# Performance work log

Measured on AMD Instinct MI355X. Metric: run time of the kernel, lower is better.

The kernel has to match this reference:

```python
import jax, jax.numpy as jnp
import numpy as np
from jax import lax

EPS = 1e-5

def conv2d(x, w, groups=1, pad=0):
    return lax.conv_general_dilated(
        x, w, window_strides=(1, 1), padding=[(pad, pad), (pad, pad)],
        dimension_numbers=('NCHW', 'OIHW', 'NCHW'), feature_group_count=groups)

def setup_inputs() -> dict:
    key = jax.random.key(0)
    ks = jax.random.split(key, 10)
    B, C, H, W = 8, 64, 128, 128
    s = 0.05
    f32 = jnp.float32
    return {
        'x': jax.random.normal(ks[0], (B, C, H, W), f32),
        # key_embed: Conv2d(64,64,3,groups=8,bias=False) -> weight [64, 64/8, 3, 3]
        'w_key': jax.random.normal(ks[1], (64, 8, 3, 3), f32) * s,
        # embed[0]: Conv2d(128,32,1,groups=2,bias=False) -> [32, 128/2, 1, 1]
        'w_e1': jax.random.normal(ks[2], (32, 64, 1, 1), f32) * s,
        # embed[2]: Conv2d(32,72,1,groups=2,bias=True) -> [72, 32/2, 1, 1]
        'w_e2': jax.random.normal(ks[3], (72, 16, 1, 1), f32) * s,
        'b_e2': jax.random.normal(ks[4], (72,), f32) * s,
        # GroupNorm(num_groups=8, num_channels=72) affine params
        'gn_w': jnp.ones((72,), f32),
        'gn_b': jnp.zeros((72,), f32),
        # conv1x1: Conv2d(64,64,1,groups=2,bias=False) -> [64, 32, 1, 1]
        'w_c1': jax.random.normal(ks[5], (64, 32, 1, 1), f32) * s,
        # conv_du: Conv2d(64,4,1,bias=False), Conv2d(4,64,1,bias=False)
        'w_du1': jax.random.normal(ks[6], (4, 64, 1, 1), f32) * s,
        'w_du2': jax.random.normal(ks[7], (64, 4, 1, 1), f32) * s,
    }

def reference(x, w_key, w_e1, w_e2, b_e2, gn_w, gn_b, w_c1, w_du1, w_du2):
    B, C, H, W = x.shape  # C == 64
    KK = 9                # kernel_size^2
    # key embedding: grouped 3x3 conv + ReLU
    k = jax.nn.relu(conv2d(x, w_key, groups=8, pad=1))
    # interleave x and k along channels: view of [B,64,2,H,W] -> [B,128,H,W]
    qk = jnp.stack([x, k], axis=2).reshape(B, 2 * C, H, W)
    # dynamic kernel generation (embed)
    w = jax.nn.relu(conv2d(qk, w_e1, groups=2))
    w = conv2d(w, w_e2, groups=2) + b_e2[None, :, None, None]  # [B,72,H,W]
    # GroupNorm(8, 72): normalize over (channels-in-group, H, W)
    wg = w.reshape(B, 8, 9, H, W)
    m = wg.mean(axis=(2, 3, 4), keepdims=True)
    v = wg.var(axis=(2, 3, 4), keepdims=True)
    w = ((wg - m) * lax.rsqrt(v + EPS)).reshape(B, 72, H, W)
    w = w * gn_w[None, :, None, None] + gn_b[None, :, None, None]
    # per-pixel kernels: [B*2, 4, 9, H, W]
    w = w.reshape(B * 2, 4, KK, H, W)
    # value path
    xv = conv2d(x, w_c1, groups=2).reshape(B * 2, 32, H, W)
    # unfold 3x3 patches with zero padding 1 -> [B*2, 32, 9, H, W]
    xp = jnp.pad(xv, ((0, 0), (0, 0), (1, 1), (1, 1)))
    patches = jnp.stack(
        [xp[:, :, i:i + H, j:j + W] for i in range(3) for j in range(3)], axis=2)
    # share_planes=8: 8 channels share each kernel -> [B*2, 4, 8, 9, H, W]
    patches = patches.reshape(B * 2, 4, 8, KK, H, W)
    out = jnp.einsum('bgckhw,bgkhw->bgchw', patches, w)  # local conv
    out = out.reshape(B, C, H, W)
    # channel attention
    y = out.mean(axis=(2, 3))                 # [B, 64]
    y = jax.nn.relu(y @ w_du1[:, :, 0, 0].T)  # [B, 4]
    y = jax.nn.sigmoid(y @ w_du2[:, :, 0, 0].T)  # [B, 64]
    return out * y[:, :, None, None]
```

## Files before the change

### kernel.cpp

```cpp
#include <hip/hip_runtime.h>
#include <math.h>

#define Hd 128
#define Wd 128
#define HW 16384

__device__ __forceinline__ float wred(float v) {
  #pragma unroll
  for (int o = 32; o > 0; o >>= 1) v += __shfl_down(v, o, 64);
  return v;
}

__global__ __launch_bounds__(256, 4) void k_fused(const float* __restrict__ x,
                                                  const float* __restrict__ wkey,
                                                  const float* __restrict__ we1,
                                                  const float* __restrict__ we2,
                                                  const float* __restrict__ be2,
                                                  const float* __restrict__ wc1,
                                                  float* __restrict__ xv,
                                                  float* __restrict__ wpre,
                                                  float* __restrict__ spart) {
  __shared__ float xt[8][18][24];
  __shared__ float sred2[4][8];
  const int tid = threadIdx.x;
  const int tx = tid & 15, ty = tid >> 4;
  const int b = blockIdx.y, s = blockIdx.z;
  const int h0 = (blockIdx.x >> 3) * 16, w0 = (blockIdx.x & 7) * 16;
  const int p = ((h0 + ty) << 7) + (w0 + tx);
  float xc[32], kc[32];
  #pragma unroll
  for (int g = 0; g < 4; ++g) {
    for (int i = tid; i < 8 * 324; i += 256) {
      int ch = i / 324, r = i - ch * 324;
      int yy = r / 18, xx = r - yy * 18;
      int gh = h0 + yy - 1, gw = w0 + xx - 1;
      float v = 0.f;
      if (gh >= 0 && gh < Hd && gw >= 0 && gw < Wd)
        v = x[((long)(b * 64 + 32 * s + 8 * g + ch) << 14) + (gh << 7) + gw];
      xt[ch][yy][xx] = v;
    }
    __syncthreads();
    float kacc[8] = {0.f, 0.f, 0.f, 0.f, 0.f, 0.f, 0.f, 0.f};
    const float* wg = wkey + (4 * s + g) * 576;
    #pragma unroll
    for (int ich = 0; ich < 8; ++ich) {
      float nb[9];
      #pragma unroll
      for (int rr = 0; rr < 3; ++rr)
        #pragma unroll
        for (int cc = 0; cc < 3; ++cc)
          nb[rr * 3 + cc] = xt[ich][ty + rr][tx + cc];
      xc[8 * g + ich] = nb[4];
      #pragma unroll
      for (int oc = 0; oc < 8; ++oc) {
        const float* wr = wg + oc * 72 + ich * 9;
        #pragma unroll
        for (int k9 = 0; k9 < 9; ++k9) kacc[oc] += wr[k9] * nb[k9];
      }
    }
    #pragma unroll
    for (int oc = 0; oc < 8; ++oc) kc[8 * g + oc] = fmaxf(kacc[oc], 0.f);
    __syncthreads();
  }
  #pragma unroll 4
  for (int o = 0; o < 32; ++o) {
    const float* wr = wc1 + (32 * s + o) * 32;
    float a = 0.f;
    #pragma unroll
    for (int j = 0; j < 32; ++j) a += wr[j] * xc[j];
    xv[((long)(b * 64 + 32 * s + o) << 14) + p] = a;
  }
  float w1a[16];
  #pragma unroll
  for (int o = 0; o < 16; ++o) {
    const float* wr = we1 + (16 * s + o) * 64;
    float a = 0.f;
    #pragma unroll
    for (int j = 0; j < 32; ++j) a += wr[2 * j] * xc[j] + wr[2 * j + 1] * kc[j];
    w1a[o] = fmaxf(a, 0.f);
  }
  #pragma unroll
  for (int gl = 0; gl < 4; ++gl) {
    float lgs = 0.f, lgq = 0.f;
    #pragma unroll
    for (int kk = 0; kk < 9; ++kk) {
      const int oc2 = 36 * s + gl * 9 + kk;
      const float* wr = we2 + oc2 * 16;
      float a = be2[oc2];
      #pragma unroll
      for (int ic = 0; ic < 16; ++ic) a += wr[ic] * w1a[ic];
      wpre[((long)(b * 72 + oc2) << 14) + p] = a;
      lgs += a;
      lgq += a * a;
    }
    float r1 = wred(lgs), r2 = wred(lgq);
    if ((tid & 63) == 0) {
      sred2[tid >> 6][2 * gl] = r1;
      sred2[tid >> 6][2 * gl + 1] = r2;
    }
  }
  __syncthreads();
  if (tid < 8) {
    float a = sred2[0][tid] + sred2[1][tid] + sred2[2][tid] + sred2[3][tid];
    spart[blockIdx.x * 128 + b * 16 + s * 8 + tid] = a;
  }
}

__global__ void k_gnstat(const float* __restrict__ spart, float* __restrict__ minv) {
  __shared__ float sred[128];
  const int t = threadIdx.x;
  float a = 0.f;
  #pragma unroll 8
  for (int r = 0; r < 64; ++r) a += spart[r * 128 + t];
  sred[t] = a;
  __syncthreads();
  if (t < 64) {
    const float N = 9.f * (float)HW;
    float s = sred[2 * t], q = sred[2 * t + 1];
    float m = s / N;
    float var = q / N - m * m;
    minv[2 * t] = m;
    minv[2 * t + 1] = rsqrtf(var + 1e-5f);
  }
}

__global__ __launch_bounds__(256) void k_local(const float* __restrict__ kxv,
                                               const float* __restrict__ wpre,
                                               const float* __restrict__ minv,
                                               const float* __restrict__ gnw,
                                               const float* __restrict__ gnb,
                                               float* __restrict__ out,
                                               float* __restrict__ part) {
  __shared__ float xt[8][34][24];
  const int tid = threadIdx.x;
  const int tx = tid & 15, ty = tid >> 4;
  const int z = blockIdx.z;
  const int b2 = z >> 2, g = z & 3;
  const int t = b2 & 1, b = b2 >> 1;
  const int h0 = blockIdx.y * 32, w0 = blockIdx.x * 16;
  for (int i = tid; i < 8 * 612; i += 256) {
    int ch = i / 612, r = i - ch * 612;
    int yy = r / 18, xx = r - yy * 18;
    int gh = h0 + yy - 1, gw = w0 + xx - 1;
    float v = 0.f;
    if (gh >= 0 && gh < Hd && gw >= 0 && gw < Wd)
      v = kxv[((long)(b2 * 32 + g * 8 + ch) << 14) + (gh << 7) + gw];
    xt[ch][yy][xx] = v;
  }
  __syncthreads();
  const int gg = 4 * t + g;
  const float m = minv[(b * 8 + gg) * 2];
  const float inv = minv[(b * 8 + gg) * 2 + 1];
  const int p0 = ((h0 + 2 * ty) << 7) + (w0 + tx);
  const int p1 = p0 + 128;
  float wn0[9], wn1[9];
  #pragma unroll
  for (int kk = 0; kk < 9; ++kk) {
    const int ch72 = 36 * t + 9 * g + kk;
    const long base = ((long)(b * 72 + ch72) << 14);
    const float sc = inv * gnw[ch72], sh = gnb[ch72] - m * inv * gnw[ch72];
    wn0[kk] = wpre[base + p0] * sc + sh;
    wn1[kk] = wpre[base + p1] * sc + sh;
  }
  const int prow = (blockIdx.y * 8 + blockIdx.x) * 4 + (tid >> 6);
  #pragma unroll
  for (int cc = 0; cc < 8; ++cc) {
    float nb[12];
    #pragma unroll
    for (int rr = 0; rr < 4; ++rr)
      #pragma unroll
      for (int ccol = 0; ccol < 3; ++ccol)
        nb[rr * 3 + ccol] = xt[cc][2 * ty + rr][tx + ccol];
    float o0 = 0.f, o1 = 0.f;
    #pragma unroll
    for (int dy = 0; dy < 3; ++dy)
      #pragma unroll
      for (int dx = 0; dx < 3; ++dx) {
        o0 += wn0[dy * 3 + dx] * nb[dy * 3 + dx];
        o1 += wn1[dy * 3 + dx] * nb[(dy + 1) * 3 + dx];
      }
    const int ch512 = b2 * 32 + g * 8 + cc;
    out[((long)ch512 << 14) + p0] = o0;
    out[((long)ch512 << 14) + p1] = o1;
    float os = wred(o0 + o1);
    if ((tid & 63) == 0) part[prow * 512 + ch512] = os;
  }
}

__global__ void k_ca(const float* __restrict__ part, const float* __restrict__ du1,
                     const float* __restrict__ du2, float* __restrict__ ys) {
  __shared__ float sy[8][64];
  __shared__ float sy4[8][4];
  const int tid = threadIdx.x;
  const int b = tid >> 6, c = tid & 63;
  float acc = 0.f;
  #pragma unroll 8
  for (int r = 0; r < 128; ++r) acc += part[r * 512 + tid];
  sy[b][c] = acc * (1.f / (float)HW);
  __syncthreads();
  if (tid < 32) {
    int bb = tid >> 2, j = tid & 3;
    float a = 0.f;
    for (int c2 = 0; c2 < 64; ++c2) a += sy[bb][c2] * du1[j * 64 + c2];
    sy4[bb][j] = fmaxf(a, 0.f);
  }
  __syncthreads();
  float z = 0.f;
  #pragma unroll
  for (int j = 0; j < 4; ++j) z += sy4[b][j] * du2[c * 4 + j];
  ys[tid] = 1.f / (1.f + expf(-z));
}

__global__ __launch_bounds__(256) void k_scale(float* __restrict__ out,
                                               const float* __restrict__ ys) {
  const long i4 = (long)blockIdx.x * 256 + threadIdx.x;
  const long e = i4 * 4;
  const int bc = (int)(e >> 14);
  const float s = ys[bc];
  float4* o = (float4*)out;
  float4 v = o[i4];
  v.x *= s; v.y *= s; v.z *= s; v.w *= s;
  o[i4] = v;
}

extern "C" void kernel_launch(void* const* d_in, const int* in_sizes, int n_in,
                              void* d_out, int out_size, void* d_ws, size_t ws_size,
                              hipStream_t stream) {
  const float* x    = (const float*)d_in[0];
  const float* wkey = (const float*)d_in[1];
  const float* we1  = (const float*)d_in[2];
  const float* we2  = (const float*)d_in[3];
  const float* be2  = (const float*)d_in[4];
  const float* gnw  = (const float*)d_in[5];
  const float* gnb  = (const float*)d_in[6];
  const float* wc1  = (const float*)d_in[7];
  const float* du1  = (const float*)d_in[8];
  const float* du2  = (const float*)d_in[9];
  float* out = (float*)d_out;
  float* ws = (float*)d_ws;

  float* kxv  = ws;
  float* wpre = ws + 8388608;
  float* part = ws + 17825792;
  float* spart = part;
  float* minv = part + 131072;
  float* ys   = minv + 128;

  k_fused<<<dim3(64, 8, 2), 256, 0, stream>>>(x, wkey, we1, we2, be2, wc1, kxv, wpre, spart);
  k_gnstat<<<1, 128, 0, stream>>>(spart, minv);
  k_local<<<dim3(8, 4, 64), 256, 0, stream>>>(kxv, wpre, minv, gnw, gnb, out, part);
  k_ca<<<1, 512, 0, stream>>>(part, du1, du2, ys);
  k_scale<<<8192, 256, 0, stream>>>(out, ys);
}
```

Measured before the change: 233.3 us.

## Store xv and wpre channel-last and fold GroupNorm stats into local conv

The intermediate value tensor xv and the pre-norm kernel tensor wpre are now stored pixel-major (channels last) instead of planar. k_fused writes xv with float4 vector stores, and k_local loads each pixel's 8 channels with two float4 loads. The separate single-block GroupNorm statistics kernel is removed: each k_local block reduces its own group's partial sums with a wavefront shuffle, which saves one launch and one serial dependency. Costs: the wpre stores and loads become strided scalar accesses of 36 floats per pixel, which may coalesce worse. The k_fused launch-bounds occupancy hint and the outer loop unroll are also dropped.

```diff
diff --git a/kernel.cpp b/kernel.cpp
--- a/kernel.cpp
+++ b/kernel.cpp
@@ -11,15 +11,15 @@
   return v;
 }
 
-__global__ __launch_bounds__(256, 4) void k_fused(const float* __restrict__ x,
-                                                  const float* __restrict__ wkey,
-                                                  const float* __restrict__ we1,
-                                                  const float* __restrict__ we2,
-                                                  const float* __restrict__ be2,
-                                                  const float* __restrict__ wc1,
-                                                  float* __restrict__ xv,
-                                                  float* __restrict__ wpre,
-                                                  float* __restrict__ spart) {
+__global__ __launch_bounds__(256) void k_fused(const float* __restrict__ x,
+                                               const float* __restrict__ wkey,
+                                               const float* __restrict__ we1,
+                                               const float* __restrict__ we2,
+                                               const float* __restrict__ be2,
+                                               const float* __restrict__ wc1,
+                                               float* __restrict__ xv,
+                                               float* __restrict__ wpre,
+                                               float* __restrict__ spart) {
   __shared__ float xt[8][18][24];
   __shared__ float sred2[4][8];
   const int tid = threadIdx.x;
@@ -28,7 +28,6 @@
   const int h0 = (blockIdx.x >> 3) * 16, w0 = (blockIdx.x & 7) * 16;
   const int p = ((h0 + ty) << 7) + (w0 + tx);
   float xc[32], kc[32];
-  #pragma unroll
   for (int g = 0; g < 4; ++g) {
     for (int i = tid; i < 8 * 324; i += 256) {
       int ch = i / 324, r = i - ch * 324;
@@ -62,13 +61,19 @@
     for (int oc = 0; oc < 8; ++oc) kc[8 * g + oc] = fmaxf(kacc[oc], 0.f);
     __syncthreads();
   }
-  #pragma unroll 4
-  for (int o = 0; o < 32; ++o) {
-    const float* wr = wc1 + (32 * s + o) * 32;
-    float a = 0.f;
-    #pragma unroll
-    for (int j = 0; j < 32; ++j) a += wr[j] * xc[j];
-    xv[((long)(b * 64 + 32 * s + o) << 14) + p] = a;
+  float* xvp = xv + ((long)(b * HW + p)) * 64 + 32 * s;
+  #pragma unroll
+  for (int o4 = 0; o4 < 8; ++o4) {
+    float va[4];
+    #pragma unroll
+    for (int oo = 0; oo < 4; ++oo) {
+      const float* wr = wc1 + (32 * s + 4 * o4 + oo) * 32;
+      float a = 0.f;
+      #pragma unroll
+      for (int j = 0; j < 32; ++j) a += wr[j] * xc[j];
+      va[oo] = a;
+    }
+    ((float4*)xvp)[o4] = make_float4(va[0], va[1], va[2], va[3]);
   }
   float w1a[16];
   #pragma unroll
@@ -79,6 +84,7 @@
     for (int j = 0; j < 32; ++j) a += wr[2 * j] * xc[j] + wr[2 * j + 1] * kc[j];
     w1a[o] = fmaxf(a, 0.f);
   }
+  float* wpp = wpre + ((long)(b * HW + p)) * 72 + 36 * s;
   #pragma unroll
   for (int gl = 0; gl < 4; ++gl) {
     float lgs = 0.f, lgq = 0.f;
@@ -89,7 +95,7 @@
       float a = be2[oc2];
       #pragma unroll
       for (int ic = 0; ic < 16; ++ic) a += wr[ic] * w1a[ic];
-      wpre[((long)(b * 72 + oc2) << 14) + p] = a;
+      wpp[gl * 9 + kk] = a;
       lgs += a;
       lgq += a * a;
     }
@@ -106,61 +112,65 @@
   }
 }
 
-__global__ void k_gnstat(const float* __restrict__ spart, float* __restrict__ minv) {
-  __shared__ float sred[128];
-  const int t = threadIdx.x;
-  float a = 0.f;
-  #pragma unroll 8
-  for (int r = 0; r < 64; ++r) a += spart[r * 128 + t];
-  sred[t] = a;
-  __syncthreads();
-  if (t < 64) {
-    const float N = 9.f * (float)HW;
-    float s = sred[2 * t], q = sred[2 * t + 1];
-    float m = s / N;
-    float var = q / N - m * m;
-    minv[2 * t] = m;
-    minv[2 * t + 1] = rsqrtf(var + 1e-5f);
-  }
-}
-
-__global__ __launch_bounds__(256) void k_local(const float* __restrict__ kxv,
+__global__ __launch_bounds__(256) void k_local(const float* __restrict__ xv,
                                                const float* __restrict__ wpre,
-                                               const float* __restrict__ minv,
+                                               const float* __restrict__ spart,
                                                const float* __restrict__ gnw,
                                                const float* __restrict__ gnb,
                                                float* __restrict__ out,
                                                float* __restrict__ part) {
   __shared__ float xt[8][34][24];
+  __shared__ float sminv[2];
   const int tid = threadIdx.x;
   const int tx = tid & 15, ty = tid >> 4;
   const int z = blockIdx.z;
   const int b2 = z >> 2, g = z & 3;
   const int t = b2 & 1, b = b2 >> 1;
+  const int gg = 4 * t + g;
   const int h0 = blockIdx.y * 32, w0 = blockIdx.x * 16;
-  for (int i = tid; i < 8 * 612; i += 256) {
-    int ch = i / 612, r = i - ch * 612;
-    int yy = r / 18, xx = r - yy * 18;
+  for (int i = tid; i < 612; i += 256) {
+    int yy = i / 18, xx = i - yy * 18;
     int gh = h0 + yy - 1, gw = w0 + xx - 1;
-    float v = 0.f;
-    if (gh >= 0 && gh < Hd && gw >= 0 && gw < Wd)
-      v = kxv[((long)(b2 * 32 + g * 8 + ch) << 14) + (gh << 7) + gw];
-    xt[ch][yy][xx] = v;
-  }
-  __syncthreads();
-  const int gg = 4 * t + g;
-  const float m = minv[(b * 8 + gg) * 2];
-  const float inv = minv[(b * 8 + gg) * 2 + 1];
+    float4 v0 = make_float4(0.f, 0.f, 0.f, 0.f), v1 = v0;
+    if (gh >= 0 && gh < Hd && gw >= 0 && gw < Wd) {
+      const float4* src = (const float4*)(xv + ((long)(b * HW) + (gh << 7) + gw) * 64 +
+                                          32 * t + 8 * g);
+      v0 = src[0];
+      v1 = src[1];
+    }
+    xt[0][yy][xx] = v0.x; xt[1][yy][xx] = v0.y; xt[2][yy][xx] = v0.z; xt[3][yy][xx] = v0.w;
+    xt[4][yy][xx] = v1.x; xt[5][yy][xx] = v1.y; xt[6][yy][xx] = v1.z; xt[7][yy][xx] = v1.w;
+  }
+  if (tid < 64) {
+    const float* sp = spart + tid * 128 + (b * 8 + gg) * 2;
+    float sv = sp[0], qv = sp[1];
+    #pragma unroll
+    for (int o = 32; o > 0; o >>= 1) {
+      sv += __shfl_down(sv, o, 64);
+      qv += __shfl_down(qv, o, 64);
+    }
+    if (tid == 0) {
+      const float N = 9.f * (float)HW;
+      float mm = sv / N;
+      float var = qv / N - mm * mm;
+      sminv[0] = mm;
+      sminv[1] = rsqrtf(var + 1e-5f);
+    }
+  }
+  __syncthreads();
+  const float m = sminv[0];
+  const float inv = sminv[1];
   const int p0 = ((h0 + 2 * ty) << 7) + (w0 + tx);
   const int p1 = p0 + 128;
+  const float* w0p = wpre + ((long)(b * HW + p0)) * 72 + 36 * t + 9 * g;
+  const float* w1p = wpre + ((long)(b * HW + p1)) * 72 + 36 * t + 9 * g;
   float wn0[9], wn1[9];
   #pragma unroll
   for (int kk = 0; kk < 9; ++kk) {
     const int ch72 = 36 * t + 9 * g + kk;
-    const long base = ((long)(b * 72 + ch72) << 14);
     const float sc = inv * gnw[ch72], sh = gnb[ch72] - m * inv * gnw[ch72];
-    wn0[kk] = wpre[base + p0] * sc + sh;
-    wn1[kk] = wpre[base + p1] * sc + sh;
+    wn0[kk] = w0p[kk] * sc + sh;
+    wn1[kk] = w1p[kk] * sc + sh;
   }
   const int prow = (blockIdx.y * 8 + blockIdx.x) * 4 + (tid >> 6);
   #pragma unroll
@@ -239,16 +249,14 @@
   float* out = (float*)d_out;
   float* ws = (float*)d_ws;
 
-  float* kxv  = ws;
+  float* xv   = ws;
   float* wpre = ws + 8388608;
   float* part = ws + 17825792;
-  float* spart = part;
-  float* minv = part + 131072;
-  float* ys   = minv + 128;
-
-  k_fused<<<dim3(64, 8, 2), 256, 0, stream>>>(x, wkey, we1, we2, be2, wc1, kxv, wpre, spart);
-  k_gnstat<<<1, 128, 0, stream>>>(spart, minv);
-  k_local<<<dim3(8, 4, 64), 256, 0, stream>>>(kxv, wpre, minv, gnw, gnb, out, part);
+  float* spart = part + 65536;
+  float* ys   = spart + 8192;
+
+  k_fused<<<dim3(64, 8, 2), 256, 0, stream>>>(x, wkey, we1, we2, be2, wc1, xv, wpre, spart);
+  k_local<<<dim3(8, 4, 64), 256, 0, stream>>>(xv, wpre, spart, gnw, gnb, out, part);
   k_ca<<<1, 512, 0, stream>>>(part, du1, du2, ys);
   k_scale<<<8192, 256, 0, stream>>>(out, ys);
 }
```

New measurement: 230.8 us. No clear change (-1.1%).
